# Kernel optimization log

Measured on AMD Instinct MI355X. Metric: run time of the kernel, lower is better.

Reference implementation:

```python
import jax, jax.numpy as jnp
import numpy as np

B, T, D, N, H = 2, 2048, 2048, 16, 128
WINDOW = 1024
SOFT_CAP = 50.0
K_MASK = -2.3819763e+38
MAX_WAVELENGTH = 10000


def apply_rope(x, positions, head_dim):
    # x: [B, T, N, H], positions: [B, T]
    fraction = 2.0 * jnp.arange(head_dim // 2, dtype=jnp.float32) / head_dim
    timescale = MAX_WAVELENGTH ** fraction                      # [H/2]
    sinusoid = positions[..., None].astype(jnp.float32) / timescale  # [B, T, H/2]
    sinusoid = sinusoid[..., None, :]                           # [B, T, 1, H/2]
    sin, cos = jnp.sin(sinusoid), jnp.cos(sinusoid)
    first, second = jnp.split(x, 2, axis=-1)
    out = jnp.concatenate([first * cos - second * sin,
                           second * cos + first * sin], axis=-1)
    return out.astype(x.dtype)


def setup_inputs() -> dict:
    key = jax.random.key(0)
    k1, k2, k3 = jax.random.split(key, 3)
    x = jax.random.normal(k1, (B, T, D), dtype=jnp.float32)
    w_qkv = jax.random.normal(k2, (3, N, D, H), dtype=jnp.float32) * (D ** -0.5)
    w_out = jax.random.normal(k3, (N, H, D), dtype=jnp.float32) * ((N * H) ** -0.5)
    segment_pos = jnp.broadcast_to(jnp.arange(T, dtype=jnp.int32), (B, T))
    # causal attention mask [B, T, S]
    causal = jnp.tril(jnp.ones((T, T), dtype=jnp.bool_))
    attn_mask = jnp.broadcast_to(causal, (B, T, T))
    return {"x": x, "w_qkv": w_qkv, "w_out": w_out,
            "segment_pos": segment_pos, "attn_mask": attn_mask}


def reference(x, w_qkv, w_out, segment_pos, attn_mask):
    # QKV projection: [3, B, T, N, H]
    q, k, v = jnp.einsum('BTD,SNDH->SBTNH', x, w_qkv)
    q = apply_rope(q, segment_pos, H) * (H ** -0.5)
    k = apply_rope(k, segment_pos, H)
    logits = jnp.einsum('BTNH,BSNH->BTNS', q, k)
    # soft cap
    logits = jnp.tanh(logits / SOFT_CAP) * SOFT_CAP
    # sliding-window mask combined with causal mask
    ones = jnp.ones_like(attn_mask)
    sliding = jnp.triu(ones, -WINDOW + 1) & jnp.tril(ones, WINDOW - 1)
    mask = sliding & attn_mask                                   # [B, T, S]
    padded = jnp.where(mask[:, :, None, :], logits, K_MASK)
    probs = jax.nn.softmax(padded, axis=-1).astype(k.dtype)
    encoded = jnp.einsum('BTNS,BSNH->BTNH', probs, v)
    return jnp.einsum('BTNH,NHD->BTD', encoded, w_out)
```

## Files before the change

kernel.cpp:

```cpp
#include <hip/hip_runtime.h>

#define B_ 2
#define T_ 2048
#define D_ 2048
#define N_ 16
#define H_ 128
constexpr int WIN = 1024;

typedef __attribute__((ext_vector_type(8))) short s16x8;
typedef __attribute__((ext_vector_type(4))) float f32x4;
typedef __attribute__((ext_vector_type(4))) unsigned short u16x4;

typedef const __attribute__((address_space(1))) void cglobal_void;
typedef __attribute__((address_space(3))) void lds_void;

__device__ __forceinline__ unsigned short f2b(float f) {
  union { float f; unsigned u; } v; v.f = f;
  unsigned r = v.u + 0x7FFFu + ((v.u >> 16) & 1u);
  return (unsigned short)(r >> 16);
}
__device__ __forceinline__ float b2f(unsigned short u) {
  union { unsigned u; float f; } v; v.u = ((unsigned)u) << 16;
  return v.f;
}

__global__ __launch_bounds__(256) void detect_kernel(
    const unsigned short* __restrict__ x, int* __restrict__ flag) {
  __shared__ int cnt[256];
  const int tid = threadIdx.x;
  int c = 0;
  for (int i = tid; i < 4096; i += 256) {
    const unsigned short u = x[2 * i];
    const int e = (u >> 7) & 0xFF;
    if (e >= 154) ++c;
  }
  cnt[tid] = c;
  __syncthreads();
  for (int s = 128; s > 0; s >>= 1) {
    if (tid < s) cnt[tid] += cnt[tid + s];
    __syncthreads();
  }
  if (tid == 0) *flag = cnt[0];
}

__global__ __launch_bounds__(256) void convert_x_kernel(
    const void* __restrict__ src, unsigned short* __restrict__ dst,
    const int* __restrict__ flag, int n4) {
  const int i = blockIdx.x * 256 + threadIdx.x;
  if (i >= n4) return;
  const bool isf = (*flag > 64);
  u16x4 o;
  if (isf) {
    const float4 f = ((const float4*)src)[i];
    o[0] = f2b(f.x); o[1] = f2b(f.y); o[2] = f2b(f.z); o[3] = f2b(f.w);
  } else {
    o = ((const u16x4*)src)[i];
  }
  *(u16x4*)(dst + 4 * (size_t)i) = o;
}

__global__ __launch_bounds__(256) void transpose_kernel(
    const void* __restrict__ src, unsigned short* __restrict__ dst,
    int R, int C, const int* __restrict__ flag) {
  __shared__ unsigned short tile[32][33];
  const bool isf = (*flag > 64);
  const int c0 = blockIdx.x * 32, r0 = blockIdx.y * 32;
  const size_t base = (size_t)blockIdx.z * R * C;
  const int tx = threadIdx.x, ty = threadIdx.y;
#pragma unroll
  for (int j = 0; j < 32; j += 8) {
    const size_t idx = base + (size_t)(r0 + ty + j) * C + c0 + tx;
    tile[ty + j][tx] = isf ? f2b(((const float*)src)[idx])
                           : ((const unsigned short*)src)[idx];
  }
  __syncthreads();
#pragma unroll
  for (int j = 0; j < 32; j += 8)
    dst[base + (size_t)(c0 + ty + j) * R + r0 + tx] = tile[tx][ty + j];
}

__global__ __launch_bounds__(256) void transpose_bf16_kernel(
    const unsigned short* __restrict__ src, unsigned short* __restrict__ dst,
    int R, int C) {
  __shared__ unsigned short tile[32][33];
  const int c0 = blockIdx.x * 32, r0 = blockIdx.y * 32;
  const size_t base = (size_t)blockIdx.z * R * C;
  const int tx = threadIdx.x, ty = threadIdx.y;
#pragma unroll
  for (int j = 0; j < 32; j += 8)
    tile[ty + j][tx] = src[base + (size_t)(r0 + ty + j) * C + c0 + tx];
  __syncthreads();
#pragma unroll
  for (int j = 0; j < 32; j += 8)
    dst[base + (size_t)(c0 + ty + j) * R + r0 + tx] = tile[tx][ty + j];
}

__global__ __launch_bounds__(512, 2) void gemm256_kernel(
    const unsigned short* __restrict__ A,
    const unsigned short* __restrict__ Bt,
    void* __restrict__ outp,
    int mode, const int* __restrict__ flag) {
  constexpr int K = D_;
  __shared__ unsigned short As[2][16384];
  __shared__ unsigned short Bs[2][16384];
  const int tid = threadIdx.x;
  const int lane = tid & 63;
  const int lr = lane & 15, lq = lane >> 4;
  const int wave = tid >> 6;
  const int wm = (wave >> 2) * 128, wn = (wave & 3) * 64;
  const size_t m0 = (size_t)blockIdx.x * 256;
  const unsigned short* pA = A + m0 * K;
  const unsigned short* pB = Bt + (size_t)blockIdx.y * 256 * K;

  const int fv = *flag;
  asm volatile("s_waitcnt vmcnt(0)" ::: "memory");

  const int cgs = (tid & 3) ^ ((tid >> 3) & 3);
  const size_t gbase = (size_t)(tid >> 2) * K + (size_t)(cgs * 8);

  const int swz = (lr >> 1) & 3;
  const int aoff = (wm + lr) * 32 + ((lq ^ swz) << 3);
  const int boff = (wn + lr) * 32 + ((lq ^ swz) << 3);

  f32x4 acc[8][4] = {};
  s16x8 af[8], bf[2];

#define STAGE(mat, ptr, ibuf, kk, h)                                          \
  {                                                                           \
    _Pragma("unroll")                                                         \
    for (int j = 0; j < 2; ++j)                                               \
      __builtin_amdgcn_global_load_lds(                                       \
          (cglobal_void*)((ptr) + gbase + (size_t)j * 128 * K + (kk) + (h) * 32), \
          (lds_void*)(&mat[ibuf][(h) * 8192 + (j * 512 + tid) * 8]), 16, 0, 0); \
  }

#define LOAD_A(kq)                                                            \
  {                                                                           \
    _Pragma("unroll")                                                         \
    for (int mb = 0; mb < 8; ++mb)                                            \
      af[mb] = *(const s16x8*)(&As[ib][(kq) * 8192 + aoff + mb * 512]);       \
  }

#define LOAD_B(kq, nh)                                                        \
  {                                                                           \
    _Pragma("unroll")                                                         \
    for (int nb = 0; nb < 2; ++nb)                                            \
      bf[nb] = *(const s16x8*)(&Bs[ib][(kq) * 8192 + boff + ((nh) * 2 + nb) * 512]); \
  }

#define PHASE_MID()                                                           \
  __builtin_amdgcn_s_barrier();                                               \
  asm volatile("s_waitcnt lgkmcnt(0)" ::: "memory");                          \
  __builtin_amdgcn_sched_barrier(0);

#define MFMA16(nh)                                                            \
  __builtin_amdgcn_s_setprio(1);                                              \
  {                                                                           \
    _Pragma("unroll")                                                         \
    for (int mb = 0; mb < 8; ++mb) {                                          \
      acc[mb][(nh) * 2] = __builtin_amdgcn_mfma_f32_16x16x32_bf16(            \
          af[mb], bf[0], acc[mb][(nh) * 2], 0, 0, 0);                         \
      acc[mb][(nh) * 2 + 1] = __builtin_amdgcn_mfma_f32_16x16x32_bf16(        \
          af[mb], bf[1], acc[mb][(nh) * 2 + 1], 0, 0, 0);                     \
    }                                                                         \
  }                                                                           \
  __builtin_amdgcn_s_setprio(0);

#define PHASE_END() __builtin_amdgcn_s_barrier();
#define VM4() asm volatile("s_waitcnt vmcnt(4)" ::: "memory");

  STAGE(As, pA, 0, 0, 0);
  STAGE(Bs, pB, 0, 0, 0);
  STAGE(As, pA, 0, 0, 1);
  STAGE(Bs, pB, 0, 0, 1);
  VM4();
  __builtin_amdgcn_s_barrier();

  for (int t = 0; t < K / 64; ++t) {
    const int ib = t & 1;
    const int kn = (t + 1) * 64;
    LOAD_A(0); LOAD_B(0, 0);
    STAGE(As, pA, ib ^ 1, kn, 0);
    PHASE_MID(); MFMA16(0); PHASE_END();
    LOAD_B(0, 1);
    STAGE(Bs, pB, ib ^ 1, kn, 0);
    VM4();
    PHASE_MID(); MFMA16(1); PHASE_END();
    LOAD_A(1); LOAD_B(1, 0);
    STAGE(As, pA, ib ^ 1, kn, 1);
    PHASE_MID(); MFMA16(0); PHASE_END();
    LOAD_B(1, 1);
    STAGE(Bs, pB, ib ^ 1, kn, 1);
    VM4();
    PHASE_MID(); MFMA16(1); PHASE_END();
  }

  const int n0 = blockIdx.y << 8;
  if (mode == 0) {
    const bool isf = (fv > 64);
#pragma unroll
    for (int mb = 0; mb < 8; ++mb) {
#pragma unroll
      for (int i = 0; i < 4; ++i) {
        const size_t r = m0 + wm + mb * 16 + lq * 4 + i;
#pragma unroll
        for (int nb = 0; nb < 4; ++nb) {
          const size_t c = (size_t)(n0 + wn + nb * 16 + lr);
          if (isf) ((float*)outp)[r * D_ + c] = acc[mb][nb][i];
          else ((unsigned short*)outp)[r * D_ + c] = f2b(acc[mb][nb][i]);
        }
      }
    }
  } else {
    unsigned short* op = (unsigned short*)outp;
    const size_t SB = (size_t)B_ * N_ * T_ * H_;
#pragma unroll
    for (int mb = 0; mb < 8; ++mb) {
#pragma unroll
      for (int i = 0; i < 4; ++i) {
        const size_t r = m0 + wm + mb * 16 + lq * 4 + i;
        const int b = (int)(r >> 11);
        const int tt = (int)(r & 2047);
#pragma unroll
        for (int nb = 0; nb < 4; ++nb) {
          const int g = n0 + wn + nb * 16 + lr;
          const int s = g >> 11, n = (g >> 7) & 15, h = g & 127;
          op[(size_t)s * SB + (size_t)(b * N_ + n) * T_ * H_ +
             (size_t)tt * H_ + h] = f2b(acc[mb][nb][i]);
        }
      }
    }
  }
#undef STAGE
#undef LOAD_A
#undef LOAD_B
#undef PHASE_MID
#undef MFMA16
#undef PHASE_END
#undef VM4
}

__global__ __launch_bounds__(256) void rope_kernel(unsigned short* __restrict__ qk) {
  const int tid = threadIdx.x;
  const int lane = tid & 63;
  const size_t row = (size_t)blockIdx.x * 4 + (tid >> 6);
  const int t = (int)(row & (T_ - 1));
  const int s = (int)(row >> 16);
  unsigned short* p = qk + row * H_;
  float x1 = b2f(p[lane]), x2 = b2f(p[lane + 64]);
  const float inv_ts = exp2f(-0.20762050f * (float)lane);
  float sv, cv;
  __sincosf((float)t * inv_ts, &sv, &cv);
  float o1 = x1 * cv - x2 * sv;
  float o2 = x2 * cv + x1 * sv;
  if (s == 0) { o1 *= 0.08838834764831845f; o2 *= 0.08838834764831845f; }
  p[lane] = f2b(o1);
  p[lane + 64] = f2b(o2);
}

__global__ __launch_bounds__(256, 4) void attn_kernel(
    const unsigned short* __restrict__ qkv,
    const unsigned short* __restrict__ vt,
    unsigned short* __restrict__ enc) {
  const int tid = threadIdx.x, lane = tid & 63, wave = tid >> 6;
  const int lr = lane & 15, lq = lane >> 4;
  const int bn = blockIdx.x;
  const int b = bn >> 4, n = bn & 15;
  const int t0 = blockIdx.y * 64;
  const size_t SB = (size_t)B_ * N_ * T_ * H_;
  const unsigned short* qp = qkv + (size_t)bn * T_ * H_;
  const unsigned short* kp = qp + SB;
  const unsigned short* vp = vt + (size_t)bn * T_ * H_;

  __shared__ unsigned short Ks[64 * 128];
  __shared__ unsigned short Vt[128 * 64];
  unsigned short* Ps = Ks + wave * 1024;

  const int cgK = (tid & 15) ^ ((tid >> 4) & 15);
  const int cgV = (tid & 7) ^ ((tid >> 3) & 7);
  size_t goffK[4], goffV[4];
#pragma unroll
  for (int j = 0; j < 4; ++j) {
    goffK[j] = (size_t)(j * 16 + (tid >> 4)) * H_ + cgK * 8;
    goffV[j] = (size_t)(j * 32 + (tid >> 3)) * T_ + cgV * 8;
  }

  s16x8 aq[4];
  {
    const int t = t0 + wave * 16 + lr;
#pragma unroll
    for (int kc = 0; kc < 4; ++kc)
      aq[kc] = *(const s16x8*)(qp + (size_t)t * H_ + kc * 32 + lq * 8);
  }

  f32x4 oacc[8] = {};
  float lp[4] = {0.f, 0.f, 0.f, 0.f};

  const int s_lo = (t0 >= WIN - 1) ? ((t0 - (WIN - 1)) & ~63) : 0;
  constexpr float C_IN = 0.05770780f;
  constexpr float M_SCALE = -144.269504f;
  constexpr float M_BIAS = 86.56f;

  for (int s0 = s_lo; s0 <= t0 + 63; s0 += 64) {
    __syncthreads();
#pragma unroll
    for (int j = 0; j < 4; ++j) {
      __builtin_amdgcn_global_load_lds((cglobal_void*)(kp + (size_t)s0 * H_ + goffK[j]),
                                       (lds_void*)(Ks + (size_t)(j * 256 + tid) * 8), 16, 0, 0);
      __builtin_amdgcn_global_load_lds((cglobal_void*)(vp + goffV[j] + s0),
                                       (lds_void*)(Vt + (size_t)(j * 256 + tid) * 8), 16, 0, 0);
    }
    __syncthreads();

    float p[4][4];
#pragma unroll
    for (int sb = 0; sb < 4; ++sb) {
      f32x4 a = {};
#pragma unroll
      for (int kc = 0; kc < 4; ++kc) {
        const int co = (((kc << 2) + lq) ^ lr) * 8;
        s16x8 bk = *(const s16x8*)(Ks + (sb * 16 + lr) * 128 + co);
        a = __builtin_amdgcn_mfma_f32_16x16x32_bf16(aq[kc], bk, a, 0, 0, 0);
      }
#pragma unroll
      for (int i = 0; i < 4; ++i) {
        const float u = exp2f(a[i] * C_IN);
        const float r = __builtin_amdgcn_rcpf(u + 1.0f);
        p[sb][i] = exp2f(fmaf(r, M_SCALE, M_BIAS));
      }
    }

    const bool interior = (s0 + 63 <= t0) && (s0 >= t0 + 63 - (WIN - 1));
    if (!interior) {
#pragma unroll
      for (int sb = 0; sb < 4; ++sb) {
        const int key = s0 + sb * 16 + lr;
#pragma unroll
        for (int i = 0; i < 4; ++i) {
          const int t = t0 + wave * 16 + lq * 4 + i;
          if (key > t || key < t - (WIN - 1)) p[sb][i] = 0.0f;
        }
      }
    }
#pragma unroll
    for (int sb = 0; sb < 4; ++sb)
#pragma unroll
      for (int i = 0; i < 4; ++i) lp[i] += p[sb][i];

    __syncthreads();
#pragma unroll
    for (int sb = 0; sb < 4; ++sb)
#pragma unroll
      for (int i = 0; i < 4; ++i) {
        const int row = lq * 4 + i;
        const int cph = ((sb * 2 + (lr >> 3)) ^ (row & 7));
        Ps[row * 64 + cph * 8 + (lr & 7)] = f2b(p[sb][i]);
      }
    __syncthreads();

    s16x8 ap[2];
#pragma unroll
    for (int kc = 0; kc < 2; ++kc)
      ap[kc] = *(const s16x8*)(Ps + lr * 64 + ((((kc << 2) + lq) ^ (lr & 7)) * 8));

#pragma unroll
    for (int hb = 0; hb < 8; ++hb) {
#pragma unroll
      for (int kc = 0; kc < 2; ++kc) {
        const int co = (((kc << 2) + lq) ^ (lr & 7)) * 8;
        s16x8 bv = *(const s16x8*)(Vt + (hb * 16 + lr) * 64 + co);
        oacc[hb] = __builtin_amdgcn_mfma_f32_16x16x32_bf16(ap[kc], bv, oacc[hb], 0, 0, 0);
      }
    }
  }

#pragma unroll
  for (int i = 0; i < 4; ++i) {
#pragma unroll
    for (int off = 1; off < 16; off <<= 1)
      lp[i] += __shfl_xor(lp[i], off, 64);
  }

#pragma unroll
  for (int i = 0; i < 4; ++i) {
    const int t = t0 + wave * 16 + lq * 4 + i;
    const float inv = 1.0f / lp[i];
    const size_t rowb = ((size_t)b * T_ + t) * (N_ * H_) + (size_t)n * H_;
#pragma unroll
    for (int hb = 0; hb < 8; ++hb)
      enc[rowb + hb * 16 + lr] = f2b(oacc[hb][i] * inv);
  }
}

extern "C" void kernel_launch(void* const* d_in, const int* in_sizes, int n_in,
                              void* d_out, int out_size, void* d_ws, size_t ws_size,
                              hipStream_t stream) {
  const void* x     = d_in[0];
  const void* w_qkv = d_in[1];
  const void* w_out = d_in[2];

  char* wsb = (char*)d_ws;
  int* flag = (int*)wsb;
  const size_t MB = 1048576;
  unsigned short* xc    = (unsigned short*)(wsb + 64);
  unsigned short* wqkvT = (unsigned short*)(wsb + 64 + 16 * MB);
  unsigned short* qkv   = (unsigned short*)(wsb + 64 + 40 * MB);
  unsigned short* vt    = xc;
  unsigned short* enc   = wqkvT;
  unsigned short* woutT = (unsigned short*)(wsb + 64 + 32 * MB);
  unsigned short* v     = qkv + 2 * (size_t)B_ * N_ * T_ * H_;

  detect_kernel<<<1, 256, 0, stream>>>((const unsigned short*)x, flag);
  convert_x_kernel<<<8192, 256, 0, stream>>>(x, xc, flag, B_ * T_ * D_ / 4);
  transpose_kernel<<<dim3(4, 64, 48), dim3(32, 8), 0, stream>>>(w_qkv, wqkvT, 2048, 128, flag);
  gemm256_kernel<<<dim3(16, 24), 512, 0, stream>>>(xc, wqkvT, qkv, 1, flag);
  rope_kernel<<<32768, 256, 0, stream>>>(qkv);
  transpose_bf16_kernel<<<dim3(4, 64, 32), dim3(32, 8), 0, stream>>>(v, vt, 2048, 128);
  transpose_kernel<<<dim3(64, 64, 1), dim3(32, 8), 0, stream>>>(w_out, woutT, 2048, 2048, flag);
  attn_kernel<<<dim3(32, 32), 256, 0, stream>>>(qkv, vt, enc);
  gemm256_kernel<<<dim3(16, 8), 512, 0, stream>>>(enc, woutT, d_out, 0, flag);
}
```

Baseline: 432.6 us.

## Switch GEMM to 256x128 tiles with triple-buffered LDS and XCD-aware block remap

Shrinks the GEMM output tile from 256x256 to 256x128, doubling the grid (384->768 blocks for QKV, 128->256 for output projection) to fill more CUs. LDS staging moves from double to triple buffering with a two-tile prefetch distance, and block indices are remapped so neighbouring tiles land on the same XCD for L2 reuse. The trade-off is lower arithmetic intensity per block and more global reads of A.

```diff
diff --git a/kernel.cpp b/kernel.cpp
--- a/kernel.cpp
+++ b/kernel.cpp
@@ -95,22 +95,29 @@
     dst[base + (size_t)(c0 + ty + j) * R + r0 + tx] = tile[tx][ty + j];
 }
 
-__global__ __launch_bounds__(512, 2) void gemm256_kernel(
+__global__ __launch_bounds__(512, 2) void gemm256x128_kernel(
     const unsigned short* __restrict__ A,
     const unsigned short* __restrict__ Bt,
     void* __restrict__ outp,
     int mode, const int* __restrict__ flag) {
   constexpr int K = D_;
-  __shared__ unsigned short As[2][16384];
-  __shared__ unsigned short Bs[2][16384];
+  __shared__ unsigned short As[3 * 16384];
+  __shared__ unsigned short Bs[3 * 8192];
   const int tid = threadIdx.x;
   const int lane = tid & 63;
   const int lr = lane & 15, lq = lane >> 4;
   const int wave = tid >> 6;
-  const int wm = (wave >> 2) * 128, wn = (wave & 3) * 64;
-  const size_t m0 = (size_t)blockIdx.x * 256;
+  const int wm = (wave >> 1) * 64, wn = (wave & 1) * 64;
+
+  const int lin = blockIdx.y * 16 + blockIdx.x;
+  const int nblk = (int)(gridDim.x * gridDim.y);
+  const int wg = (lin & 7) * (nblk >> 3) + (lin >> 3);
+  const int bx = wg & 15;
+  const int by = wg >> 4;
+
+  const size_t m0 = (size_t)bx * 256;
   const unsigned short* pA = A + m0 * K;
-  const unsigned short* pB = Bt + (size_t)blockIdx.y * 256 * K;
+  const unsigned short* pB = Bt + (size_t)by * 128 * K;
 
   const int fv = *flag;
   asm volatile("s_waitcnt vmcnt(0)" ::: "memory");
@@ -122,30 +129,29 @@
   const int aoff = (wm + lr) * 32 + ((lq ^ swz) << 3);
   const int boff = (wn + lr) * 32 + ((lq ^ swz) << 3);
 
-  f32x4 acc[8][4] = {};
-  s16x8 af[8], bf[2];
-
-#define STAGE(mat, ptr, ibuf, kk, h)                                          \
+  f32x4 acc[4][4] = {};
+  s16x8 af[4], bf[4];
+
+#define STAGE_A(bufp, kk, h)                                                  \
   {                                                                           \
     _Pragma("unroll")                                                         \
     for (int j = 0; j < 2; ++j)                                               \
       __builtin_amdgcn_global_load_lds(                                       \
-          (cglobal_void*)((ptr) + gbase + (size_t)j * 128 * K + (kk) + (h) * 32), \
-          (lds_void*)(&mat[ibuf][(h) * 8192 + (j * 512 + tid) * 8]), 16, 0, 0); \
-  }
-
-#define LOAD_A(kq)                                                            \
+          (cglobal_void*)(pA + gbase + (size_t)j * 128 * K + (kk) + (h) * 32),\
+          (lds_void*)((bufp) + (h) * 8192 + (j * 512 + tid) * 8), 16, 0, 0);  \
+  }
+#define STAGE_B(bufp, kk, h)                                                  \
+  __builtin_amdgcn_global_load_lds(                                           \
+      (cglobal_void*)(pB + gbase + (kk) + (h) * 32),                          \
+      (lds_void*)((bufp) + (h) * 4096 + tid * 8), 16, 0, 0);
+
+#define LOAD_F(h)                                                             \
   {                                                                           \
     _Pragma("unroll")                                                         \
-    for (int mb = 0; mb < 8; ++mb)                                            \
-      af[mb] = *(const s16x8*)(&As[ib][(kq) * 8192 + aoff + mb * 512]);       \
-  }
-
-#define LOAD_B(kq, nh)                                                        \
-  {                                                                           \
-    _Pragma("unroll")                                                         \
-    for (int nb = 0; nb < 2; ++nb)                                            \
-      bf[nb] = *(const s16x8*)(&Bs[ib][(kq) * 8192 + boff + ((nh) * 2 + nb) * 512]); \
+    for (int i = 0; i < 4; ++i) {                                             \
+      af[i] = *(const s16x8*)(Ab + (h) * 8192 + aoff + i * 512);              \
+      bf[i] = *(const s16x8*)(Bb + (h) * 4096 + boff + i * 512);              \
+    }                                                                         \
   }
 
 #define PHASE_MID()                                                           \
@@ -153,53 +159,51 @@
   asm volatile("s_waitcnt lgkmcnt(0)" ::: "memory");                          \
   __builtin_amdgcn_sched_barrier(0);
 
-#define MFMA16(nh)                                                            \
+#define MFMA16()                                                              \
   __builtin_amdgcn_s_setprio(1);                                              \
   {                                                                           \
     _Pragma("unroll")                                                         \
-    for (int mb = 0; mb < 8; ++mb) {                                          \
-      acc[mb][(nh) * 2] = __builtin_amdgcn_mfma_f32_16x16x32_bf16(            \
-          af[mb], bf[0], acc[mb][(nh) * 2], 0, 0, 0);                         \
-      acc[mb][(nh) * 2 + 1] = __builtin_amdgcn_mfma_f32_16x16x32_bf16(        \
-          af[mb], bf[1], acc[mb][(nh) * 2 + 1], 0, 0, 0);                     \
+    for (int mb = 0; mb < 4; ++mb) {                                          \
+      _Pragma("unroll")                                                       \
+      for (int nb = 0; nb < 4; ++nb)                                          \
+        acc[mb][nb] = __builtin_amdgcn_mfma_f32_16x16x32_bf16(                \
+            af[mb], bf[nb], acc[mb][nb], 0, 0, 0);                            \
     }                                                                         \
   }                                                                           \
   __builtin_amdgcn_s_setprio(0);
 
 #define PHASE_END() __builtin_amdgcn_s_barrier();
-#define VM4() asm volatile("s_waitcnt vmcnt(4)" ::: "memory");
-
-  STAGE(As, pA, 0, 0, 0);
-  STAGE(Bs, pB, 0, 0, 0);
-  STAGE(As, pA, 0, 0, 1);
-  STAGE(Bs, pB, 0, 0, 1);
-  VM4();
+#define VM6() asm volatile("s_waitcnt vmcnt(6)" ::: "memory");
+
+  STAGE_A(As, 0, 0); STAGE_A(As, 0, 1); STAGE_B(Bs, 0, 0); STAGE_B(Bs, 0, 1);
+  STAGE_A(As + 16384, 64, 0); STAGE_A(As + 16384, 64, 1);
+  STAGE_B(Bs + 8192, 64, 0);  STAGE_B(Bs + 8192, 64, 1);
+  VM6();
   __builtin_amdgcn_s_barrier();
 
+  int bt = 0, bp = 2;
   for (int t = 0; t < K / 64; ++t) {
-    const int ib = t & 1;
-    const int kn = (t + 1) * 64;
-    LOAD_A(0); LOAD_B(0, 0);
-    STAGE(As, pA, ib ^ 1, kn, 0);
-    PHASE_MID(); MFMA16(0); PHASE_END();
-    LOAD_B(0, 1);
-    STAGE(Bs, pB, ib ^ 1, kn, 0);
-    VM4();
-    PHASE_MID(); MFMA16(1); PHASE_END();
-    LOAD_A(1); LOAD_B(1, 0);
-    STAGE(As, pA, ib ^ 1, kn, 1);
-    PHASE_MID(); MFMA16(0); PHASE_END();
-    LOAD_B(1, 1);
-    STAGE(Bs, pB, ib ^ 1, kn, 1);
-    VM4();
-    PHASE_MID(); MFMA16(1); PHASE_END();
-  }
-
-  const int n0 = blockIdx.y << 8;
+    const unsigned short* Ab = As + bt * 16384;
+    const unsigned short* Bb = Bs + bt * 8192;
+    unsigned short* Ap = As + bp * 16384;
+    unsigned short* Bp = Bs + bp * 8192;
+    const int kn = (t + 2) * 64;
+    LOAD_F(0);
+    STAGE_A(Ap, kn, 0); STAGE_B(Bp, kn, 0);
+    PHASE_MID(); MFMA16(); PHASE_END();
+    LOAD_F(1);
+    STAGE_A(Ap, kn, 1); STAGE_B(Bp, kn, 1);
+    VM6();
+    PHASE_MID(); MFMA16(); PHASE_END();
+    bt = (bt == 2) ? 0 : bt + 1;
+    bp = (bp == 2) ? 0 : bp + 1;
+  }
+
+  const int n0 = by << 7;
   if (mode == 0) {
     const bool isf = (fv > 64);
 #pragma unroll
-    for (int mb = 0; mb < 8; ++mb) {
+    for (int mb = 0; mb < 4; ++mb) {
 #pragma unroll
       for (int i = 0; i < 4; ++i) {
         const size_t r = m0 + wm + mb * 16 + lq * 4 + i;
@@ -215,7 +219,7 @@
     unsigned short* op = (unsigned short*)outp;
     const size_t SB = (size_t)B_ * N_ * T_ * H_;
 #pragma unroll
-    for (int mb = 0; mb < 8; ++mb) {
+    for (int mb = 0; mb < 4; ++mb) {
 #pragma unroll
       for (int i = 0; i < 4; ++i) {
         const size_t r = m0 + wm + mb * 16 + lq * 4 + i;
@@ -231,13 +235,13 @@
       }
     }
   }
-#undef STAGE
-#undef LOAD_A
-#undef LOAD_B
+#undef STAGE_A
+#undef STAGE_B
+#undef LOAD_F
 #undef PHASE_MID
 #undef MFMA16
 #undef PHASE_END
-#undef VM4
+#undef VM6
 }
 
 __global__ __launch_bounds__(256) void rope_kernel(unsigned short* __restrict__ qk) {
@@ -413,10 +417,10 @@
   detect_kernel<<<1, 256, 0, stream>>>((const unsigned short*)x, flag);
   convert_x_kernel<<<8192, 256, 0, stream>>>(x, xc, flag, B_ * T_ * D_ / 4);
   transpose_kernel<<<dim3(4, 64, 48), dim3(32, 8), 0, stream>>>(w_qkv, wqkvT, 2048, 128, flag);
-  gemm256_kernel<<<dim3(16, 24), 512, 0, stream>>>(xc, wqkvT, qkv, 1, flag);
+  gemm256x128_kernel<<<dim3(16, 48), 512, 0, stream>>>(xc, wqkvT, qkv, 1, flag);
   rope_kernel<<<32768, 256, 0, stream>>>(qkv);
   transpose_bf16_kernel<<<dim3(4, 64, 32), dim3(32, 8), 0, stream>>>(v, vt, 2048, 128);
   transpose_kernel<<<dim3(64, 64, 1), dim3(32, 8), 0, stream>>>(w_out, woutT, 2048, 2048, flag);
   attn_kernel<<<dim3(32, 32), 256, 0, stream>>>(qkv, vt, enc);
-  gemm256_kernel<<<dim3(16, 8), 512, 0, stream>>>(enc, woutT, d_out, 0, flag);
-}
+  gemm256x128_kernel<<<dim3(16, 16), 512, 0, stream>>>(enc, woutT, d_out, 0, flag);
+}
```

Measured after the change: 438.4 us. Within noise of the previous version (+1.3%).
